# Kernel optimization log

Measured on AMD Instinct MI355X. Metric: run time of the kernel, lower is better.

The kernel has to match this reference:

```python
import jax, jax.numpy as jnp
import numpy as np

N_NODES = 4096
N_EDGES = 8192
N_GRAPHS = 256
D_NODE = 64
D_EDGE = 32
H = 256


def setup_inputs() -> dict:
    key = jax.random.key(0)
    ks = jax.random.split(key, 16)
    s = lambda d: 1.0 / np.sqrt(d)
    inp = {
        "x": jax.random.normal(ks[0], (N_NODES, D_NODE), dtype=jnp.float32),
        "edge_index": jax.random.randint(ks[1], (2, N_EDGES), 0, N_NODES),
        "edge_attr": jax.random.normal(ks[2], (N_EDGES, D_EDGE), dtype=jnp.float32),
        "batch": jnp.sort(jax.random.randint(ks[3], (N_NODES,), 0, N_GRAPHS)),
        # conv1: edge MLP 32 -> 64*256, root weight 64->256, bias 256
        "nn1_w": jax.random.normal(ks[4], (D_EDGE, D_NODE * H), dtype=jnp.float32) * s(D_EDGE),
        "nn1_b": jnp.zeros((D_NODE * H,), dtype=jnp.float32),
        "root1_w": jax.random.normal(ks[5], (D_NODE, H), dtype=jnp.float32) * s(D_NODE),
        "bias1": jnp.zeros((H,), dtype=jnp.float32),
        # conv2: edge MLP 32 -> 256*256, root weight 256->256, bias 256
        "nn2_w": jax.random.normal(ks[6], (D_EDGE, H * H), dtype=jnp.float32) * s(D_EDGE),
        "nn2_b": jnp.zeros((H * H,), dtype=jnp.float32),
        "root2_w": jax.random.normal(ks[7], (H, H), dtype=jnp.float32) * s(H),
        "bias2": jnp.zeros((H,), dtype=jnp.float32),
        # readout MLP: 256 -> 128 -> 1
        "lin1_w": jax.random.normal(ks[8], (H, H // 2), dtype=jnp.float32) * s(H),
        "lin1_b": jnp.zeros((H // 2,), dtype=jnp.float32),
        "lin2_w": jax.random.normal(ks[9], (H // 2, 1), dtype=jnp.float32) * s(H // 2),
        "lin2_b": jnp.zeros((1,), dtype=jnp.float32),
    }
    return inp


def nnconv(x, src, dst, edge_attr, nn_w, nn_b, root_w, bias, out_c):
    # PyG NNConv (aggr='add'): per-edge weight matrix from edge MLP,
    # message = x[src] @ W_e, scatter-add at dst, plus root transform + bias.
    e = edge_attr.shape[0]
    in_c = x.shape[1]
    w_e = (edge_attr @ nn_w + nn_b).reshape(e, in_c, out_c)  # [E, in, out]
    msg = jnp.einsum('ei,eio->eo', x[src], w_e)              # [E, out]
    agg = jax.ops.segment_sum(msg, dst, num_segments=x.shape[0])
    return agg + x @ root_w + bias


def reference(x, edge_index, edge_attr, batch,
              nn1_w, nn1_b, root1_w, bias1,
              nn2_w, nn2_b, root2_w, bias2,
              lin1_w, lin1_b, lin2_w, lin2_b):
    src, dst = edge_index[0], edge_index[1]
    h = nnconv(x, src, dst, edge_attr, nn1_w, nn1_b, root1_w, bias1, H)
    h = jax.nn.relu(h)
    h = nnconv(h, src, dst, edge_attr, nn2_w, nn2_b, root2_w, bias2, H)
    # global mean pool over graphs
    sums = jax.ops.segment_sum(h, batch, num_segments=N_GRAPHS)
    cnts = jax.ops.segment_sum(jnp.ones((h.shape[0],), h.dtype), batch, num_segments=N_GRAPHS)
    pooled = sums / jnp.maximum(cnts, 1.0)[:, None]
    # dropout is identity in eval mode
    z = jax.nn.relu(pooled @ lin1_w + lin1_b)
    return jax.nn.sigmoid(z @ lin2_w + lin2_b)  # [N_GRAPHS, 1]
```

## Files before the change

### kernel.cpp

```cpp
#include <hip/hip_runtime.h>
#include <math.h>

#define N_NODES 4096
#define N_EDGES 8192
#define N_GRAPHS 256
#define D_NODE 64
#define D_EDGE 32
#define HH 256

#define K1 2176
#define K2 8704
#define NSL1 8
#define NSL2 12

typedef _Float16 half8v __attribute__((ext_vector_type(8)));
typedef _Float16 half4v __attribute__((ext_vector_type(4)));
typedef float floatx4 __attribute__((ext_vector_type(4)));

static const size_t OFF_S    = 0;
static const size_t OFF_BT1  = 17825792;
static const size_t OFF_BT2  = 18104320;
static const size_t OFF_CP   = 19218432;
static const size_t OFF_H    = 25509888;
static const size_t OFF_INT  = 26034176;

__device__ void csr_body(const int* __restrict__ dst,
                         int* __restrict__ starts,
                         int* __restrict__ elist) {
    __shared__ int cnt[4096];
    __shared__ int ps[256];
    int t = threadIdx.x;
#pragma unroll
    for (int i = 0; i < 16; ++i) cnt[t * 16 + i] = 0;
    __syncthreads();
#pragma unroll
    for (int i = 0; i < 32; ++i) atomicAdd(&cnt[dst[i * 256 + t]], 1);
    __syncthreads();
    int v[16]; int s = 0;
#pragma unroll
    for (int i = 0; i < 16; ++i) { v[i] = cnt[t * 16 + i]; s += v[i]; }
    ps[t] = s;
    __syncthreads();
    for (int off = 1; off < 256; off <<= 1) {
        int tv = (t >= off) ? ps[t - off] : 0;
        __syncthreads();
        ps[t] += tv;
        __syncthreads();
    }
    int excl = ps[t] - s;
#pragma unroll
    for (int i = 0; i < 16; ++i) {
        starts[t * 16 + i] = excl;
        cnt[t * 16 + i] = excl;
        excl += v[i];
    }
    if (t == 255) starts[4096] = excl;
    __syncthreads();
#pragma unroll
    for (int i = 0; i < 32; ++i) {
        int e = i * 256 + t;
        int d = dst[e];
        int p = atomicAdd(&cnt[d], 1);
        elist[p] = e;
    }
}

__device__ void packT_body(const float* __restrict__ w,
                           const float* __restrict__ b,
                           const float* __restrict__ rw,
                           _Float16* __restrict__ BT,
                           int kk0, int o0, int K,
                           int wlim, int blim, int wshift, int wmask, int wrow) {
    __shared__ float T[64][65];
    int t = threadIdx.x;
    int ol = t & 63, kb = t >> 6;
#pragma unroll
    for (int p = 0; p < 16; ++p) {
        int kl = p * 4 + kb;
        int kk = kk0 + kl, o = o0 + ol;
        float v;
        if (kk < wlim)      v = w[(kk >> wshift) * wrow + (kk & wmask) * 256 + o];
        else if (kk < blim) v = b[(kk - wlim) * 256 + o];
        else                v = rw[(kk - blim) * 256 + o];
        T[kl][ol] = v;
    }
    __syncthreads();
    int kl2 = t & 63, ob = t >> 6;
#pragma unroll
    for (int p = 0; p < 16; ++p) {
        int ol2 = p * 4 + ob;
        BT[(size_t)(o0 + ol2) * K + kk0 + kl2] = (_Float16)T[kl2][ol2];
    }
}

__global__ __launch_bounds__(256) void prep_k(const int* __restrict__ dst,
                                              int* __restrict__ starts,
                                              int* __restrict__ elist,
                                              const float* __restrict__ w1,
                                              const float* __restrict__ b1,
                                              const float* __restrict__ r1,
                                              const float* __restrict__ w2,
                                              const float* __restrict__ b2,
                                              const float* __restrict__ r2,
                                              _Float16* __restrict__ BT1,
                                              _Float16* __restrict__ BT2) {
    int bx = blockIdx.x, by = blockIdx.y;
    if (bx == 0) {
        if (by == 0) csr_body(dst, starts, elist);
        return;
    }
    int pbx = bx - 1, o0 = by * 64;
    if (pbx < K1 / 64)
        packT_body(w1, b1, r1, BT1, pbx * 64, o0, K1, 2048, 2112, 6, 63, 16384);
    else
        packT_body(w2, b2, r2, BT2, (pbx - K1 / 64) * 64, o0, K2, 8192, 8448, 8, 255, 65536);
}

__global__ __launch_bounds__(64) void s1_k(const float* __restrict__ x,
                                           const float* __restrict__ ea,
                                           const int* __restrict__ src,
                                           const int* __restrict__ starts,
                                           const int* __restrict__ elist,
                                           _Float16* __restrict__ S) {
    int n = blockIdx.x, t = threadIdx.x;
    int cg = t & 7, kg = t >> 3;
    int i0 = cg * 8;
    float acc[5][8] = {};
    int e0 = starts[n], e1 = starts[n + 1];
    for (int ie = e0; ie < e1; ++ie) {
        int e = elist[ie];
        int sn = src[e];
        float4 f0 = *(const float4*)&x[sn * 64 + i0];
        float4 f1 = *(const float4*)&x[sn * 64 + i0 + 4];
        float xv[8] = {f0.x, f0.y, f0.z, f0.w, f1.x, f1.y, f1.z, f1.w};
#pragma unroll
        for (int j = 0; j < 4; ++j) {
            float va = ea[e * 32 + kg + 8 * j];
#pragma unroll
            for (int c = 0; c < 8; ++c) acc[j][c] += va * xv[c];
        }
        if (kg == 0) {
#pragma unroll
            for (int c = 0; c < 8; ++c) acc[4][c] += xv[c];
        }
    }
    _Float16* row = S + (size_t)n * K1;
#pragma unroll
    for (int j = 0; j < 4; ++j) {
        int k = kg + 8 * j;
        half8v o;
#pragma unroll
        for (int c = 0; c < 8; ++c) o[c] = (_Float16)acc[j][c];
        *(half8v*)&row[k * 64 + i0] = o;
    }
    if (kg == 0) {
        half8v o;
#pragma unroll
        for (int c = 0; c < 8; ++c) o[c] = (_Float16)acc[4][c];
        *(half8v*)&row[32 * 64 + i0] = o;
    }
    if (kg == 1) {
        float4 f0 = *(const float4*)&x[n * 64 + i0];
        float4 f1 = *(const float4*)&x[n * 64 + i0 + 4];
        half8v o;
        o[0] = (_Float16)f0.x; o[1] = (_Float16)f0.y; o[2] = (_Float16)f0.z; o[3] = (_Float16)f0.w;
        o[4] = (_Float16)f1.x; o[5] = (_Float16)f1.y; o[6] = (_Float16)f1.z; o[7] = (_Float16)f1.w;
        *(half8v*)&row[2112 + i0] = o;
    }
}

__global__ __launch_bounds__(256) void s2_k(const _Float16* __restrict__ h,
                                            const float* __restrict__ ea,
                                            const int* __restrict__ src,
                                            const int* __restrict__ starts,
                                            const int* __restrict__ elist,
                                            _Float16* __restrict__ S) {
    int n = blockIdx.x, t = threadIdx.x;
    int cg = t & 31, kg = t >> 5;
    int i0 = cg * 8;
    float acc[5][8] = {};
    int e0 = starts[n], e1 = starts[n + 1];
    for (int ie = e0; ie < e1; ++ie) {
        int e = elist[ie];
        int sn = src[e];
        half8v hv = *(const half8v*)&h[sn * 256 + i0];
        float xv[8];
#pragma unroll
        for (int c = 0; c < 8; ++c) xv[c] = (float)hv[c];
#pragma unroll
        for (int j = 0; j < 4; ++j) {
            float va = ea[e * 32 + kg + 8 * j];
#pragma unroll
            for (int c = 0; c < 8; ++c) acc[j][c] += va * xv[c];
        }
        if (kg == 0) {
#pragma unroll
            for (int c = 0; c < 8; ++c) acc[4][c] += xv[c];
        }
    }
    _Float16* row = S + (size_t)n * K2;
#pragma unroll
    for (int j = 0; j < 4; ++j) {
        int k = kg + 8 * j;
        half8v o;
#pragma unroll
        for (int c = 0; c < 8; ++c) o[c] = (_Float16)acc[j][c];
        *(half8v*)&row[k * 256 + i0] = o;
    }
    if (kg == 0) {
        half8v o;
#pragma unroll
        for (int c = 0; c < 8; ++c) o[c] = (_Float16)acc[4][c];
        *(half8v*)&row[32 * 256 + i0] = o;
    }
    if (kg == 1) {
        half8v hv = *(const half8v*)&h[n * 256 + i0];
        *(half8v*)&row[8448 + i0] = hv;
    }
}

__device__ __forceinline__ void async_copy16(const void* g, void* l) {
    __builtin_amdgcn_global_load_lds(
        (__attribute__((address_space(1))) unsigned int*)(g),
        (__attribute__((address_space(3))) unsigned int*)(l), 16, 0, 0);
}

__global__ __launch_bounds__(256, 3) void gemm_f16(const _Float16* __restrict__ A,
                                                   const _Float16* __restrict__ BT,
                                                   _Float16* __restrict__ Cpart,
                                                   int K, int NC, int Z) {
    __shared__ _Float16 lds[17408];
    _Float16* As = lds;
    _Float16* Bs = lds + 128 * 64;
    int tid = threadIdx.x;
    int w = tid >> 6, l = tid & 63;
    int mt = blockIdx.y, nt = blockIdx.x, z = blockIdx.z;
    int c0 = z * NC / Z, c1 = (z + 1) * NC / Z;
    int k0 = c0 * 64;
    int wm = w & 1, wn = w >> 1;

    int lr = l >> 3, lc = l & 7;
    int gc = lc ^ lr;
    const _Float16* gA0 = A  + (size_t)(mt * 128 + w * 32 + lr) * K + k0 + gc * 8;
    const _Float16* gB0 = BT + (size_t)(nt * 128 + w * 32 + lr) * K + k0 + gc * 8;

    int lm = l & 15, q4 = l >> 4;
    int sw = lm & 7;

    floatx4 acc[4][4] = {};

    for (int s = c0; s < c1; ++s) {
#pragma unroll
        for (int q = 0; q < 4; ++q) {
            async_copy16(gA0 + (size_t)q * 8 * K, As + (w * 32 + q * 8) * 64);
            async_copy16(gB0 + (size_t)q * 8 * K, Bs + (w * 32 + q * 8) * 64);
        }
        gA0 += 64; gB0 += 64;
        __syncthreads();
#pragma unroll
        for (int kw = 0; kw < 2; ++kw) {
            int ck = ((kw * 4 + q4) ^ sw) * 8;
            half8v af[4], bf[4];
#pragma unroll
            for (int i = 0; i < 4; ++i)
                af[i] = *(const half8v*)&As[(wm * 64 + i * 16 + lm) * 64 + ck];
#pragma unroll
            for (int j = 0; j < 4; ++j)
                bf[j] = *(const half8v*)&Bs[(wn * 64 + j * 16 + lm) * 64 + ck];
#pragma unroll
            for (int i = 0; i < 4; ++i)
#pragma unroll
                for (int j = 0; j < 4; ++j)
                    acc[i][j] = __builtin_amdgcn_mfma_f32_16x16x32_f16(af[i], bf[j], acc[i][j], 0, 0, 0);
        }
        __syncthreads();
    }

    _Float16* ep = lds + w * 4352;
#pragma unroll
    for (int i = 0; i < 4; ++i)
#pragma unroll
        for (int j = 0; j < 4; ++j)
#pragma unroll
            for (int r = 0; r < 4; ++r)
                ep[(i * 16 + q4 * 4 + r) * 68 + j * 16 + lm] = (_Float16)acc[i][j][r];
    __syncthreads();
    _Float16* Cp = Cpart + (size_t)z * (N_NODES * HH);
    int row8 = l >> 3, colg = (l & 7) * 8;
    int gm0 = mt * 128 + wm * 64, gn0 = nt * 128 + wn * 64;
#pragma unroll
    for (int i8 = 0; i8 < 8; ++i8) {
        int rr = i8 * 8 + row8;
        half4v lo = *(const half4v*)&ep[rr * 68 + colg];
        half4v hi = *(const half4v*)&ep[rr * 68 + colg + 4];
        half8v v;
        v[0] = lo[0]; v[1] = lo[1]; v[2] = lo[2]; v[3] = lo[3];
        v[4] = hi[0]; v[5] = hi[1]; v[6] = hi[2]; v[7] = hi[3];
        *(half8v*)&Cp[(size_t)(gm0 + rr) * HH + gn0 + colg] = v;
    }
}

__global__ __launch_bounds__(256) void hep_k(const _Float16* __restrict__ Cp,
                                             const float* __restrict__ bias,
                                             _Float16* __restrict__ h) {
    int idx = (blockIdx.x * 256 + threadIdx.x) * 8;
    float a[8] = {};
#pragma unroll
    for (int zz = 0; zz < NSL1; ++zz) {
        half8v v = *(const half8v*)(Cp + (size_t)zz * (N_NODES * HH) + idx);
#pragma unroll
        for (int j = 0; j < 8; ++j) a[j] += (float)v[j];
    }
    int col = idx & 255;
    half8v o;
#pragma unroll
    for (int j = 0; j < 8; ++j) o[j] = (_Float16)fmaxf(a[j] + bias[col + j], 0.f);
    *(half8v*)(h + idx) = o;
}

__global__ __launch_bounds__(256) void poolread_k(const _Float16* __restrict__ Cp,
                                                  const int* __restrict__ batch,
                                                  const float* __restrict__ bias2,
                                                  const float* __restrict__ l1w,
                                                  const float* __restrict__ l1b,
                                                  const float* __restrict__ l2w,
                                                  const float* __restrict__ l2b,
                                                  float* __restrict__ out) {
    int g = blockIdx.x, t = threadIdx.x;
    __shared__ int bnds[2];
    __shared__ float sp[256];
    __shared__ float sz[128];
    if (t < 2) {
        int target = g + t;
        int lo = 0, hi = N_NODES;
        while (lo < hi) { int mid = (lo + hi) >> 1; if (batch[mid] < target) lo = mid + 1; else hi = mid; }
        bnds[t] = lo;
    }
    __syncthreads();
    int lo = bnds[0], hi = bnds[1];
    float s = 0.f;
    for (int n = lo; n < hi; ++n) {
#pragma unroll
        for (int zz = 0; zz < NSL2; ++zz)
            s += (float)Cp[(size_t)zz * (N_NODES * HH) + (size_t)n * HH + t];
    }
    sp[t] = (hi > lo) ? (s / (float)(hi - lo) + bias2[t]) : 0.f;
    __syncthreads();
    if (t < 128) {
        float a = l1b[t];
#pragma unroll 8
        for (int i = 0; i < 256; ++i) a += sp[i] * l1w[i * 128 + t];
        sz[t] = fmaxf(a, 0.f) * l2w[t];
    }
    __syncthreads();
    for (int ss = 64; ss > 0; ss >>= 1) {
        if (t < ss) sz[t] += sz[t + ss];
        __syncthreads();
    }
    if (t == 0) {
        float zz = sz[0] + l2b[0];
        out[g] = 1.0f / (1.0f + expf(-zz));
    }
}

extern "C" void kernel_launch(void* const* d_in, const int* in_sizes, int n_in,
                              void* d_out, int out_size, void* d_ws, size_t ws_size,
                              hipStream_t stream) {
    const float* x       = (const float*)d_in[0];
    const int*   ei      = (const int*)d_in[1];
    const float* ea      = (const float*)d_in[2];
    const int*   batch   = (const int*)d_in[3];
    const float* nn1_w   = (const float*)d_in[4];
    const float* nn1_b   = (const float*)d_in[5];
    const float* root1_w = (const float*)d_in[6];
    const float* bias1   = (const float*)d_in[7];
    const float* nn2_w   = (const float*)d_in[8];
    const float* nn2_b   = (const float*)d_in[9];
    const float* root2_w = (const float*)d_in[10];
    const float* bias2   = (const float*)d_in[11];
    const float* lin1_w  = (const float*)d_in[12];
    const float* lin1_b  = (const float*)d_in[13];
    const float* lin2_w  = (const float*)d_in[14];
    const float* lin2_b  = (const float*)d_in[15];
    float* out = (float*)d_out;
    float* ws  = (float*)d_ws;

    _Float16* S   = (_Float16*)(ws + OFF_S);
    _Float16* BT1 = (_Float16*)(ws + OFF_BT1);
    _Float16* BT2 = (_Float16*)(ws + OFF_BT2);
    _Float16* Cp  = (_Float16*)(ws + OFF_CP);
    _Float16* h   = (_Float16*)(ws + OFF_H);
    int* ip     = (int*)(ws + OFF_INT);
    int* starts = ip;
    int* elist  = ip + 4100;

    const int* srcv = ei;
    const int* dstv = ei + N_EDGES;

    prep_k<<<dim3(1 + K1 / 64 + K2 / 64, 4), 256, 0, stream>>>(
        dstv, starts, elist, nn1_w, nn1_b, root1_w, nn2_w, nn2_b, root2_w, BT1, BT2);

    s1_k<<<4096, 64, 0, stream>>>(x, ea, srcv, starts, elist, S);

    gemm_f16<<<dim3(2, 32, NSL1), 256, 0, stream>>>(S, BT1, Cp, K1, K1 / 64, NSL1);

    hep_k<<<512, 256, 0, stream>>>(Cp, bias1, h);

    s2_k<<<4096, 256, 0, stream>>>(h, ea, srcv, starts, elist, S);

    gemm_f16<<<dim3(2, 32, NSL2), 256, 0, stream>>>(S, BT2, Cp, K2, K2 / 64, NSL2);

    poolread_k<<<N_GRAPHS, 256, 0, stream>>>(Cp, batch, bias2,
                                             lin1_w, lin1_b, lin2_w, lin2_b, out);
}
```

Before: 196.0 us.

## Fuse edge-feature gather into GEMM A-tile construction, dropping S materialization

Removes the separate s1/s2 kernels that wrote the large fp16 S matrix to global memory. Each GEMM block now builds its A tile on the fly by gathering neighbor features and edge attributes per node and K-chunk, accumulating in fp32, then writing the result to LDS. This cuts the global write and read of S and two launches. In exchange the gather is recomputed for each of the two N-tiles and costs many scattered loads and VALU work inside the GEMM loop, which can stall the MFMA pipeline.

```diff
diff --git a/kernel.cpp b/kernel.cpp
--- a/kernel.cpp
+++ b/kernel.cpp
@@ -10,14 +10,16 @@
 
 #define K1 2176
 #define K2 8704
+#define NC1 34
+#define NC2 136
 #define NSL1 8
 #define NSL2 12
+#define MAXD 8
 
 typedef _Float16 half8v __attribute__((ext_vector_type(8)));
 typedef _Float16 half4v __attribute__((ext_vector_type(4)));
 typedef float floatx4 __attribute__((ext_vector_type(4)));
 
-static const size_t OFF_S    = 0;
 static const size_t OFF_BT1  = 17825792;
 static const size_t OFF_BT2  = 18104320;
 static const size_t OFF_CP   = 19218432;
@@ -110,113 +112,10 @@
         return;
     }
     int pbx = bx - 1, o0 = by * 64;
-    if (pbx < K1 / 64)
+    if (pbx < NC1)
         packT_body(w1, b1, r1, BT1, pbx * 64, o0, K1, 2048, 2112, 6, 63, 16384);
     else
-        packT_body(w2, b2, r2, BT2, (pbx - K1 / 64) * 64, o0, K2, 8192, 8448, 8, 255, 65536);
-}
-
-__global__ __launch_bounds__(64) void s1_k(const float* __restrict__ x,
-                                           const float* __restrict__ ea,
-                                           const int* __restrict__ src,
-                                           const int* __restrict__ starts,
-                                           const int* __restrict__ elist,
-                                           _Float16* __restrict__ S) {
-    int n = blockIdx.x, t = threadIdx.x;
-    int cg = t & 7, kg = t >> 3;
-    int i0 = cg * 8;
-    float acc[5][8] = {};
-    int e0 = starts[n], e1 = starts[n + 1];
-    for (int ie = e0; ie < e1; ++ie) {
-        int e = elist[ie];
-        int sn = src[e];
-        float4 f0 = *(const float4*)&x[sn * 64 + i0];
-        float4 f1 = *(const float4*)&x[sn * 64 + i0 + 4];
-        float xv[8] = {f0.x, f0.y, f0.z, f0.w, f1.x, f1.y, f1.z, f1.w};
-#pragma unroll
-        for (int j = 0; j < 4; ++j) {
-            float va = ea[e * 32 + kg + 8 * j];
-#pragma unroll
-            for (int c = 0; c < 8; ++c) acc[j][c] += va * xv[c];
-        }
-        if (kg == 0) {
-#pragma unroll
-            for (int c = 0; c < 8; ++c) acc[4][c] += xv[c];
-        }
-    }
-    _Float16* row = S + (size_t)n * K1;
-#pragma unroll
-    for (int j = 0; j < 4; ++j) {
-        int k = kg + 8 * j;
-        half8v o;
-#pragma unroll
-        for (int c = 0; c < 8; ++c) o[c] = (_Float16)acc[j][c];
-        *(half8v*)&row[k * 64 + i0] = o;
-    }
-    if (kg == 0) {
-        half8v o;
-#pragma unroll
-        for (int c = 0; c < 8; ++c) o[c] = (_Float16)acc[4][c];
-        *(half8v*)&row[32 * 64 + i0] = o;
-    }
-    if (kg == 1) {
-        float4 f0 = *(const float4*)&x[n * 64 + i0];
-        float4 f1 = *(const float4*)&x[n * 64 + i0 + 4];
-        half8v o;
-        o[0] = (_Float16)f0.x; o[1] = (_Float16)f0.y; o[2] = (_Float16)f0.z; o[3] = (_Float16)f0.w;
-        o[4] = (_Float16)f1.x; o[5] = (_Float16)f1.y; o[6] = (_Float16)f1.z; o[7] = (_Float16)f1.w;
-        *(half8v*)&row[2112 + i0] = o;
-    }
-}
-
-__global__ __launch_bounds__(256) void s2_k(const _Float16* __restrict__ h,
-                                            const float* __restrict__ ea,
-                                            const int* __restrict__ src,
-                                            const int* __restrict__ starts,
-                                            const int* __restrict__ elist,
-                                            _Float16* __restrict__ S) {
-    int n = blockIdx.x, t = threadIdx.x;
-    int cg = t & 31, kg = t >> 5;
-    int i0 = cg * 8;
-    float acc[5][8] = {};
-    int e0 = starts[n], e1 = starts[n + 1];
-    for (int ie = e0; ie < e1; ++ie) {
-        int e = elist[ie];
-        int sn = src[e];
-        half8v hv = *(const half8v*)&h[sn * 256 + i0];
-        float xv[8];
-#pragma unroll
-        for (int c = 0; c < 8; ++c) xv[c] = (float)hv[c];
-#pragma unroll
-        for (int j = 0; j < 4; ++j) {
-            float va = ea[e * 32 + kg + 8 * j];
-#pragma unroll
-            for (int c = 0; c < 8; ++c) acc[j][c] += va * xv[c];
-        }
-        if (kg == 0) {
-#pragma unroll
-            for (int c = 0; c < 8; ++c) acc[4][c] += xv[c];
-        }
-    }
-    _Float16* row = S + (size_t)n * K2;
-#pragma unroll
-    for (int j = 0; j < 4; ++j) {
-        int k = kg + 8 * j;
-        half8v o;
-#pragma unroll
-        for (int c = 0; c < 8; ++c) o[c] = (_Float16)acc[j][c];
-        *(half8v*)&row[k * 256 + i0] = o;
-    }
-    if (kg == 0) {
-        half8v o;
-#pragma unroll
-        for (int c = 0; c < 8; ++c) o[c] = (_Float16)acc[4][c];
-        *(half8v*)&row[32 * 256 + i0] = o;
-    }
-    if (kg == 1) {
-        half8v hv = *(const half8v*)&h[n * 256 + i0];
-        *(half8v*)&row[8448 + i0] = hv;
-    }
+        packT_body(w2, b2, r2, BT2, (pbx - NC1) * 64, o0, K2, 8192, 8448, 8, 255, 65536);
 }
 
 __device__ __forceinline__ void async_copy16(const void* g, void* l) {
@@ -225,10 +124,16 @@
         (__attribute__((address_space(3))) unsigned int*)(l), 16, 0, 0);
 }
 
-__global__ __launch_bounds__(256, 3) void gemm_f16(const _Float16* __restrict__ A,
-                                                   const _Float16* __restrict__ BT,
-                                                   _Float16* __restrict__ Cpart,
-                                                   int K, int NC, int Z) {
+template<int CONV>
+__global__ __launch_bounds__(256, 3) void gemm_fused(const float* __restrict__ x,
+                                                     const _Float16* __restrict__ hm,
+                                                     const float* __restrict__ ea,
+                                                     const int* __restrict__ src,
+                                                     const int* __restrict__ starts,
+                                                     const int* __restrict__ elist,
+                                                     const _Float16* __restrict__ BT,
+                                                     _Float16* __restrict__ Cpart,
+                                                     int K, int NC, int Z) {
     __shared__ _Float16 lds[17408];
     _Float16* As = lds;
     _Float16* Bs = lds + 128 * 64;
@@ -239,23 +144,120 @@
     int k0 = c0 * 64;
     int wm = w & 1, wn = w >> 1;
 
-    int lr = l >> 3, lc = l & 7;
-    int gc = lc ^ lr;
-    const _Float16* gA0 = A  + (size_t)(mt * 128 + w * 32 + lr) * K + k0 + gc * 8;
+    int lr = l >> 3, lc = l & 7, gc = lc ^ lr;
     const _Float16* gB0 = BT + (size_t)(nt * 128 + w * 32 + lr) * K + k0 + gc * 8;
 
-    int lm = l & 15, q4 = l >> 4;
-    int sw = lm & 7;
+    int br = tid >> 1, bh = tid & 1;
+    int node = mt * 128 + br;
+    int e0 = starts[node], e1 = starts[node + 1];
+    int dc = e1 - e0; if (dc > MAXD) dc = MAXD;
+    int ec[MAXD], sc[MAXD];
+#pragma unroll
+    for (int d = 0; d < MAXD; ++d) {
+        if (d < dc) { int e = elist[e0 + d]; ec[d] = e; sc[d] = src[e]; }
+        else        { ec[d] = 0; sc[d] = 0; }
+    }
+    _Float16* arow = As + br * 64;
+    int rsw = br & 7;
+
+    int lm = l & 15, q4 = l >> 4, sw = lm & 7;
 
     floatx4 acc[4][4] = {};
 
     for (int s = c0; s < c1; ++s) {
 #pragma unroll
-        for (int q = 0; q < 4; ++q) {
-            async_copy16(gA0 + (size_t)q * 8 * K, As + (w * 32 + q * 8) * 64);
+        for (int q = 0; q < 4; ++q)
             async_copy16(gB0 + (size_t)q * 8 * K, Bs + (w * 32 + q * 8) * 64);
+        gB0 += 64;
+
+        float a0[32];
+        if (CONV == 1) {
+            if (s < 33) {
+                int k = s;
+#pragma unroll
+                for (int c = 0; c < 32; ++c) a0[c] = 0.f;
+#pragma unroll
+                for (int d = 0; d < MAXD; ++d) {
+                    if (d < dc) {
+                        float va = (k == 32) ? 1.f : ea[ec[d] * 32 + k];
+                        const float4* xp = (const float4*)&x[(size_t)sc[d] * 64 + bh * 32];
+#pragma unroll
+                        for (int g = 0; g < 8; ++g) {
+                            float4 f = xp[g];
+                            a0[g * 4 + 0] += va * f.x; a0[g * 4 + 1] += va * f.y;
+                            a0[g * 4 + 2] += va * f.z; a0[g * 4 + 3] += va * f.w;
+                        }
+                    }
+                }
+                for (int ie = e0 + MAXD; ie < e1; ++ie) {
+                    int e = elist[ie]; int sn = src[e];
+                    float va = (k == 32) ? 1.f : ea[e * 32 + k];
+                    const float4* xp = (const float4*)&x[(size_t)sn * 64 + bh * 32];
+#pragma unroll
+                    for (int g = 0; g < 8; ++g) {
+                        float4 f = xp[g];
+                        a0[g * 4 + 0] += va * f.x; a0[g * 4 + 1] += va * f.y;
+                        a0[g * 4 + 2] += va * f.z; a0[g * 4 + 3] += va * f.w;
+                    }
+                }
+            } else {
+                const float4* xp = (const float4*)&x[(size_t)node * 64 + bh * 32];
+#pragma unroll
+                for (int g = 0; g < 8; ++g) {
+                    float4 f = xp[g];
+                    a0[g * 4 + 0] = f.x; a0[g * 4 + 1] = f.y;
+                    a0[g * 4 + 2] = f.z; a0[g * 4 + 3] = f.w;
+                }
+            }
+        } else {
+            if (s < 132) {
+                int k = s >> 2, ib = (s & 3) * 64;
+#pragma unroll
+                for (int c = 0; c < 32; ++c) a0[c] = 0.f;
+#pragma unroll
+                for (int d = 0; d < MAXD; ++d) {
+                    if (d < dc) {
+                        float va = (k == 32) ? 1.f : ea[ec[d] * 32 + k];
+                        const half8v* hp = (const half8v*)&hm[(size_t)sc[d] * 256 + ib + bh * 32];
+#pragma unroll
+                        for (int g = 0; g < 4; ++g) {
+                            half8v hv = hp[g];
+#pragma unroll
+                            for (int c = 0; c < 8; ++c) a0[g * 8 + c] += va * (float)hv[c];
+                        }
+                    }
+                }
+                for (int ie = e0 + MAXD; ie < e1; ++ie) {
+                    int e = elist[ie]; int sn = src[e];
+                    float va = (k == 32) ? 1.f : ea[e * 32 + k];
+                    const half8v* hp = (const half8v*)&hm[(size_t)sn * 256 + ib + bh * 32];
+#pragma unroll
+                    for (int g = 0; g < 4; ++g) {
+                        half8v hv = hp[g];
+#pragma unroll
+                        for (int c = 0; c < 8; ++c) a0[g * 8 + c] += va * (float)hv[c];
+                    }
+                }
+            } else {
+                int ib = (s - 132) * 64;
+                const half8v* hp = (const half8v*)&hm[(size_t)node * 256 + ib + bh * 32];
+#pragma unroll
+                for (int g = 0; g < 4; ++g) {
+                    half8v hv = hp[g];
+#pragma unroll
+                    for (int c = 0; c < 8; ++c) a0[g * 8 + c] = (float)hv[c];
+                }
+            }
         }
-        gA0 += 64; gB0 += 64;
+
+#pragma unroll
+        for (int g = 0; g < 4; ++g) {
+            half8v o;
+#pragma unroll
+            for (int c = 0; c < 8; ++c) o[c] = (_Float16)a0[g * 8 + c];
+            *(half8v*)&arow[((bh * 4 + g) ^ rsw) * 8] = o;
+        }
+
         __syncthreads();
 #pragma unroll
         for (int kw = 0; kw < 2; ++kw) {
@@ -385,7 +387,6 @@
     float* out = (float*)d_out;
     float* ws  = (float*)d_ws;
 
-    _Float16* S   = (_Float16*)(ws + OFF_S);
     _Float16* BT1 = (_Float16*)(ws + OFF_BT1);
     _Float16* BT2 = (_Float16*)(ws + OFF_BT2);
     _Float16* Cp  = (_Float16*)(ws + OFF_CP);
@@ -397,18 +398,16 @@
     const int* srcv = ei;
     const int* dstv = ei + N_EDGES;
 
-    prep_k<<<dim3(1 + K1 / 64 + K2 / 64, 4), 256, 0, stream>>>(
+    prep_k<<<dim3(1 + NC1 + NC2, 4), 256, 0, stream>>>(
         dstv, starts, elist, nn1_w, nn1_b, root1_w, nn2_w, nn2_b, root2_w, BT1, BT2);
 
-    s1_k<<<4096, 64, 0, stream>>>(x, ea, srcv, starts, elist, S);
-
-    gemm_f16<<<dim3(2, 32, NSL1), 256, 0, stream>>>(S, BT1, Cp, K1, K1 / 64, NSL1);
+    gemm_fused<1><<<dim3(2, 32, NSL1), 256, 0, stream>>>(
+        x, h, ea, srcv, starts, elist, BT1, Cp, K1, NC1, NSL1);
 
     hep_k<<<512, 256, 0, stream>>>(Cp, bias1, h);
 
-    s2_k<<<4096, 256, 0, stream>>>(h, ea, srcv, starts, elist, S);
-
-    gemm_f16<<<dim3(2, 32, NSL2), 256, 0, stream>>>(S, BT2, Cp, K2, K2 / 64, NSL2);
+    gemm_fused<2><<<dim3(2, 32, NSL2), 256, 0, stream>>>(
+        x, h, ea, srcv, starts, elist, BT2, Cp, K2, NC2, NSL2);
 
     poolread_k<<<N_GRAPHS, 256, 0, stream>>>(Cp, batch, bias2,
                                              lin1_w, lin1_b, lin2_w, lin2_b, out);
```

Result: slower. 280.1 us (+42.9%).

## Fuse graph mean-pool into second GEMM epilogue via segmented atomic accumulation

Applied to the files above, without the earlier changes.

The second split-K GEMM no longer writes its 12 fp16 partial slices to global memory. Its epilogue does a run-length segmented sum over rows grouped by graph id and atomically adds the results into a float pool buffer. That buffer is zeroed inside hep_k, and the readout kernel just divides by the count. This removes the large partial-output write and its re-read in the pooling kernel. In exchange it adds float atomics, a serial 64-row loop per thread in the epilogue, and nondeterministic summation order.

```diff
diff --git a/kernel.cpp b/kernel.cpp
--- a/kernel.cpp
+++ b/kernel.cpp
@@ -23,6 +23,7 @@
 static const size_t OFF_CP   = 19218432;
 static const size_t OFF_H    = 25509888;
 static const size_t OFF_INT  = 26034176;
+static const size_t OFF_POOL = 26050560;
 
 __device__ void csr_body(const int* __restrict__ dst,
                          int* __restrict__ starts,
@@ -225,11 +226,15 @@
         (__attribute__((address_space(3))) unsigned int*)(l), 16, 0, 0);
 }
 
+template<int POOL>
 __global__ __launch_bounds__(256, 3) void gemm_f16(const _Float16* __restrict__ A,
                                                    const _Float16* __restrict__ BT,
                                                    _Float16* __restrict__ Cpart,
+                                                   const int* __restrict__ batch,
+                                                   float* __restrict__ pool,
                                                    int K, int NC, int Z) {
     __shared__ _Float16 lds[17408];
+    __shared__ int gids[128];
     _Float16* As = lds;
     _Float16* Bs = lds + 128 * 64;
     int tid = threadIdx.x;
@@ -284,25 +289,46 @@
 #pragma unroll
             for (int r = 0; r < 4; ++r)
                 ep[(i * 16 + q4 * 4 + r) * 68 + j * 16 + lm] = (_Float16)acc[i][j][r];
-    __syncthreads();
-    _Float16* Cp = Cpart + (size_t)z * (N_NODES * HH);
-    int row8 = l >> 3, colg = (l & 7) * 8;
-    int gm0 = mt * 128 + wm * 64, gn0 = nt * 128 + wn * 64;
-#pragma unroll
-    for (int i8 = 0; i8 < 8; ++i8) {
-        int rr = i8 * 8 + row8;
-        half4v lo = *(const half4v*)&ep[rr * 68 + colg];
-        half4v hi = *(const half4v*)&ep[rr * 68 + colg + 4];
-        half8v v;
-        v[0] = lo[0]; v[1] = lo[1]; v[2] = lo[2]; v[3] = lo[3];
-        v[4] = hi[0]; v[5] = hi[1]; v[6] = hi[2]; v[7] = hi[3];
-        *(half8v*)&Cp[(size_t)(gm0 + rr) * HH + gn0 + colg] = v;
+    if (POOL == 1 && tid < 128) gids[tid] = batch[mt * 128 + tid];
+    __syncthreads();
+
+    int gn0 = nt * 128 + wn * 64;
+    if (POOL == 0) {
+        _Float16* Cp = Cpart + (size_t)z * (N_NODES * HH);
+        int row8 = l >> 3, colg = (l & 7) * 8;
+        int gm0 = mt * 128 + wm * 64;
+#pragma unroll
+        for (int i8 = 0; i8 < 8; ++i8) {
+            int rr = i8 * 8 + row8;
+            half4v lo = *(const half4v*)&ep[rr * 68 + colg];
+            half4v hi = *(const half4v*)&ep[rr * 68 + colg + 4];
+            half8v v;
+            v[0] = lo[0]; v[1] = lo[1]; v[2] = lo[2]; v[3] = lo[3];
+            v[4] = hi[0]; v[5] = hi[1]; v[6] = hi[2]; v[7] = hi[3];
+            *(half8v*)&Cp[(size_t)(gm0 + rr) * HH + gn0 + colg] = v;
+        }
+    } else {
+        int gbase = wm * 64;
+        int gprev = gids[gbase];
+        float run = 0.f;
+        for (int rr = 0; rr < 64; ++rr) {
+            float v = (float)ep[rr * 68 + l];
+            int g = gids[gbase + rr];
+            if (g != gprev) {
+                atomicAdd(&pool[gprev * 256 + gn0 + l], run);
+                run = 0.f; gprev = g;
+            }
+            run += v;
+        }
+        atomicAdd(&pool[gprev * 256 + gn0 + l], run);
     }
 }
 
 __global__ __launch_bounds__(256) void hep_k(const _Float16* __restrict__ Cp,
                                              const float* __restrict__ bias,
-                                             _Float16* __restrict__ h) {
+                                             _Float16* __restrict__ h,
+                                             float* __restrict__ pool) {
+    if (blockIdx.x < 256) pool[blockIdx.x * 256 + threadIdx.x] = 0.f;
     int idx = (blockIdx.x * 256 + threadIdx.x) * 8;
     float a[8] = {};
 #pragma unroll
@@ -318,14 +344,14 @@
     *(half8v*)(h + idx) = o;
 }
 
-__global__ __launch_bounds__(256) void poolread_k(const _Float16* __restrict__ Cp,
-                                                  const int* __restrict__ batch,
-                                                  const float* __restrict__ bias2,
-                                                  const float* __restrict__ l1w,
-                                                  const float* __restrict__ l1b,
-                                                  const float* __restrict__ l2w,
-                                                  const float* __restrict__ l2b,
-                                                  float* __restrict__ out) {
+__global__ __launch_bounds__(256) void readout_k(const float* __restrict__ pool,
+                                                 const int* __restrict__ batch,
+                                                 const float* __restrict__ bias2,
+                                                 const float* __restrict__ l1w,
+                                                 const float* __restrict__ l1b,
+                                                 const float* __restrict__ l2w,
+                                                 const float* __restrict__ l2b,
+                                                 float* __restrict__ out) {
     int g = blockIdx.x, t = threadIdx.x;
     __shared__ int bnds[2];
     __shared__ float sp[256];
@@ -338,13 +364,7 @@
     }
     __syncthreads();
     int lo = bnds[0], hi = bnds[1];
-    float s = 0.f;
-    for (int n = lo; n < hi; ++n) {
-#pragma unroll
-        for (int zz = 0; zz < NSL2; ++zz)
-            s += (float)Cp[(size_t)zz * (N_NODES * HH) + (size_t)n * HH + t];
-    }
-    sp[t] = (hi > lo) ? (s / (float)(hi - lo) + bias2[t]) : 0.f;
+    sp[t] = (hi > lo) ? (pool[g * 256 + t] / (float)(hi - lo) + bias2[t]) : 0.f;
     __syncthreads();
     if (t < 128) {
         float a = l1b[t];
@@ -393,6 +413,7 @@
     int* ip     = (int*)(ws + OFF_INT);
     int* starts = ip;
     int* elist  = ip + 4100;
+    float* pool = ws + OFF_POOL;
 
     const int* srcv = ei;
     const int* dstv = ei + N_EDGES;
@@ -402,14 +423,14 @@
 
     s1_k<<<4096, 64, 0, stream>>>(x, ea, srcv, starts, elist, S);
 
-    gemm_f16<<<dim3(2, 32, NSL1), 256, 0, stream>>>(S, BT1, Cp, K1, K1 / 64, NSL1);
-
-    hep_k<<<512, 256, 0, stream>>>(Cp, bias1, h);
+    gemm_f16<0><<<dim3(2, 32, NSL1), 256, 0, stream>>>(S, BT1, Cp, batch, pool, K1, K1 / 64, NSL1);
+
+    hep_k<<<512, 256, 0, stream>>>(Cp, bias1, h, pool);
 
     s2_k<<<4096, 256, 0, stream>>>(h, ea, srcv, starts, elist, S);
 
-    gemm_f16<<<dim3(2, 32, NSL2), 256, 0, stream>>>(S, BT2, Cp, K2, K2 / 64, NSL2);
-
-    poolread_k<<<N_GRAPHS, 256, 0, stream>>>(Cp, batch, bias2,
-                                             lin1_w, lin1_b, lin2_w, lin2_b, out);
-}
+    gemm_f16<1><<<dim3(2, 32, NSL2), 256, 0, stream>>>(S, BT2, Cp, batch, pool, K2, K2 / 64, NSL2);
+
+    readout_k<<<N_GRAPHS, 256, 0, stream>>>(pool, batch, bias2,
+                                            lin1_w, lin1_b, lin2_w, lin2_b, out);
+}
```

Result: faster. 185.1 us (-5.6%).
